# Kernel tuning notes

Measured on AMD Instinct MI355X. Metric: run time of the kernel, lower is better.

## Reference

```python
import jax, jax.numpy as jnp
import numpy as np

N, E = 50000, 800000
IN, HID, H, C = 128, 64, 4, 2
NEG_SLOPE = 0.2


def _gat_layer(h, src, dst, W, al, ar, b, out_dim, residual, resW=None, act='elu'):
    # h: [N, in]; W: [H*out, in]; al/ar: [H, out]; b: [H*out]
    n = h.shape[0]
    feat = (h @ W.T).reshape(n, H, out_dim)            # [N, H, out]
    el = jnp.einsum('nho,ho->nh', feat, al)            # [N, H]
    er = jnp.einsum('nho,ho->nh', feat, ar)            # [N, H]
    e = jax.nn.leaky_relu(el[src] + er[dst], NEG_SLOPE)  # [E, H]
    # segment softmax over incoming edges of each dst node
    emax = jax.ops.segment_max(e, dst, num_segments=n)
    ee = jnp.exp(e - emax[dst])
    denom = jax.ops.segment_sum(ee, dst, num_segments=n)
    alpha = ee / denom[dst]                             # [E, H]
    msg = feat[src] * alpha[:, :, None]                 # [E, H, out]
    rst = jax.ops.segment_sum(msg, dst, num_segments=n)  # [N, H, out]
    if residual == 'id':
        rst = rst + h.reshape(n, H, out_dim)
    elif residual == 'fc':
        rst = rst + (h @ resW.T).reshape(n, H, out_dim)
    rst = rst + b.reshape(1, H, out_dim)
    if act == 'elu':
        rst = jax.nn.elu(rst)
    else:  # softmax over last dim (F.softmax)
        rst = jax.nn.softmax(rst, axis=-1)
    return rst


def setup_inputs() -> dict:
    key = jax.random.key(0)
    ks = jax.random.split(key, 24)
    x = jax.random.normal(ks[0], (N, IN), dtype=jnp.float32)
    src = jax.random.randint(ks[1], (E,), 0, N)
    dst = jax.random.randint(ks[2], (E,), 0, N)
    s = 0.1
    d = {'x': x, 'src': src, 'dst': dst}
    # layer 1: IN -> (H, HID), no residual
    d['W1'] = jax.random.normal(ks[3], (H * HID, IN), dtype=jnp.float32) * s
    d['al1'] = jax.random.normal(ks[4], (H, HID), dtype=jnp.float32) * s
    d['ar1'] = jax.random.normal(ks[5], (H, HID), dtype=jnp.float32) * s
    d['b1'] = jnp.zeros((H * HID,), dtype=jnp.float32)
    # layers 2,3: H*HID -> (H, HID), identity residual
    d['W2'] = jax.random.normal(ks[6], (H * HID, H * HID), dtype=jnp.float32) * s
    d['al2'] = jax.random.normal(ks[7], (H, HID), dtype=jnp.float32) * s
    d['ar2'] = jax.random.normal(ks[8], (H, HID), dtype=jnp.float32) * s
    d['b2'] = jnp.zeros((H * HID,), dtype=jnp.float32)
    d['W3'] = jax.random.normal(ks[9], (H * HID, H * HID), dtype=jnp.float32) * s
    d['al3'] = jax.random.normal(ks[10], (H, HID), dtype=jnp.float32) * s
    d['ar3'] = jax.random.normal(ks[11], (H, HID), dtype=jnp.float32) * s
    d['b3'] = jnp.zeros((H * HID,), dtype=jnp.float32)
    # layer 4: H*HID -> (H, C), linear residual, softmax activation, mean over heads
    d['W4'] = jax.random.normal(ks[12], (H * C, H * HID), dtype=jnp.float32) * s
    d['al4'] = jax.random.normal(ks[13], (H, C), dtype=jnp.float32) * s
    d['ar4'] = jax.random.normal(ks[14], (H, C), dtype=jnp.float32) * s
    d['b4'] = jnp.zeros((H * C,), dtype=jnp.float32)
    d['resW4'] = jax.random.normal(ks[15], (H * C, H * HID), dtype=jnp.float32) * s
    return d


def reference(x, src, dst, W1, al1, ar1, b1, W2, al2, ar2, b2, W3, al3, ar3, b3, W4, al4, ar4, b4, resW4):
    h = _gat_layer(x, src, dst, W1, al1, ar1, b1, HID, 'none', act='elu').reshape(N, H * HID)
    h = _gat_layer(h, src, dst, W2, al2, ar2, b2, HID, 'id', act='elu').reshape(N, H * HID)
    h = _gat_layer(h, src, dst, W3, al3, ar3, b3, HID, 'id', act='elu').reshape(N, H * HID)
    h = _gat_layer(h, src, dst, W4, al4, ar4, b4, C, 'fc', resW=resW4, act='softmax')
    return h.mean(axis=1)  # [N, C]
```

## Files before the change

### kernel.cpp

```cpp
#include <hip/hip_runtime.h>
#include <hip/hip_bf16.h>
#include <math.h>


#define LEAKY_SLOPE 0.2f

typedef __bf16 bf16x8_t __attribute__((ext_vector_type(8)));
typedef float f32x4_t __attribute__((ext_vector_type(4)));
typedef float f32x2_t __attribute__((ext_vector_type(2)));

__device__ __forceinline__ float leaky(float x) { return x > 0.f ? x : LEAKY_SLOPE * x; }
__device__ __forceinline__ float eluf(float x)  { return x > 0.f ? x : expm1f(x); }
__device__ __forceinline__ float bflo(unsigned u) { return __uint_as_float(u << 16); }
__device__ __forceinline__ float bfhi(unsigned u) { return __uint_as_float(u & 0xffff0000u); }
__device__ __forceinline__ unsigned pk2(float a, float b) {
  __hip_bfloat162 t;
  t.x = __float2bfloat16(a);
  t.y = __float2bfloat16(b);
  return *(unsigned*)&t;
}

__device__ __forceinline__ float rlf(float v, int l) {
  return __uint_as_float((unsigned)__builtin_amdgcn_readlane((int)__float_as_uint(v), l));
}
template <int CTRL>
__device__ __forceinline__ float dpp_add(float x) {
  int t = __builtin_amdgcn_update_dpp(0, (int)__float_as_uint(x), CTRL, 0xf, 0xf, false);
  return x + __uint_as_float((unsigned)t);
}
__device__ __forceinline__ float wsum_dpp(float x) {
  x = dpp_add<0x111>(x);
  x = dpp_add<0x112>(x);
  x = dpp_add<0x114>(x);
  x = dpp_add<0x118>(x);
  x = dpp_add<0x142>(x);
  x = dpp_add<0x143>(x);
  return rlf(x, 63);
}
__device__ __forceinline__ float rowsum_dpp(float x) {
  x = dpp_add<0x111>(x);
  x = dpp_add<0x112>(x);
  x = dpp_add<0x114>(x);
  x = dpp_add<0x118>(x);
  return x;
}
__device__ __forceinline__ float wmax(float v) {
#pragma unroll
  for (int o = 32; o; o >>= 1) v = fmaxf(v, __shfl_xor(v, o));
  return v;
}
__device__ __forceinline__ float wsum_sh(float v) {
#pragma unroll
  for (int o = 32; o; o >>= 1) v += __shfl_xor(v, o);
  return v;
}

__device__ __forceinline__ void quad_fma(f32x2_t& a0, f32x2_t& a1, f32x2_t& a2, f32x2_t& a3,
                                         uint4 u, float w) {
  f32x2_t wv = {w, w};
  f32x2_t f;
  f[0] = bflo(u.x); f[1] = bfhi(u.x); a0 = __builtin_elementwise_fma(wv, f, a0);
  f[0] = bflo(u.y); f[1] = bfhi(u.y); a1 = __builtin_elementwise_fma(wv, f, a1);
  f[0] = bflo(u.z); f[1] = bfhi(u.z); a2 = __builtin_elementwise_fma(wv, f, a2);
  f[0] = bflo(u.w); f[1] = bfhi(u.w); a3 = __builtin_elementwise_fma(wv, f, a3);
}

__device__ __forceinline__ void gl_lds16(const __hip_bfloat16* g, __bf16* l) {
  __builtin_amdgcn_global_load_lds((const __attribute__((address_space(1))) void*)g,
                                   (__attribute__((address_space(3))) void*)l, 16, 0, 0);
}

__global__ __launch_bounds__(1024) void scan1_k(const int* __restrict__ deg,
                                                int* __restrict__ rowp,
                                                int* __restrict__ bsum, int n) {
  __shared__ int wtot[16];
  __shared__ int wpre[16];
  int tid = threadIdx.x, lane = tid & 63, wid = tid >> 6;
  int i = blockIdx.x * 1024 + tid;
  int v = (i < n) ? deg[i] : 0;
  int x = v;
#pragma unroll
  for (int off = 1; off < 64; off <<= 1) {
    int t = __shfl_up(x, off);
    if (lane >= off) x += t;
  }
  if (lane == 63) wtot[wid] = x;
  __syncthreads();
  if (wid == 0 && lane < 16) {
    int s = wtot[lane];
    int y = s;
#pragma unroll
    for (int off = 1; off < 16; off <<= 1) {
      int t = __shfl_up(y, off);
      if (lane >= off) y += t;
    }
    wpre[lane] = y - s;
    if (lane == 15) bsum[blockIdx.x] = y;
  }
  __syncthreads();
  if (i < n) rowp[i] = wpre[wid] + x - v;
}

__global__ void scan23_k(const int* __restrict__ bsum, int* __restrict__ rowp, int n, int nb) {
  __shared__ int pref[65];
  int tid = threadIdx.x;
  if (tid < 64) {
    int v = (tid < nb) ? bsum[tid] : 0;
    int x = v;
#pragma unroll
    for (int off = 1; off < 64; off <<= 1) {
      int t = __shfl_up(x, off);
      if (tid >= off) x += t;
    }
    pref[tid] = x - v;
    if (tid == 63) pref[64] = x;
  }
  __syncthreads();
  int i = blockIdx.x * 256 + tid;
  if (i < n) rowp[i] += pref[i >> 10];
  if (i == n) rowp[n] = pref[64];
}

__global__ void scatter_k(const int* __restrict__ src, const int* __restrict__ dst,
                          const int* __restrict__ rowp, int* __restrict__ cur,
                          int* __restrict__ csrc, int e) {
  int i = blockIdx.x * 256 + threadIdx.x;
  if (i < e) {
    int d = dst[i];
    int p = atomicAdd(&cur[d], 1);
    csrc[rowp[d] + p] = src[i];
  }
}

__global__ void cvthist_k(const float* __restrict__ x, const float* __restrict__ W1,
                          const float* __restrict__ W2, const float* __restrict__ W3,
                          const float* __restrict__ W4, const float* __restrict__ rW4,
                          __hip_bfloat16* __restrict__ xb, __hip_bfloat16* __restrict__ W1b,
                          __hip_bfloat16* __restrict__ W2b, __hip_bfloat16* __restrict__ W3b,
                          __hip_bfloat16* __restrict__ Wcatb, int nx4,
                          const int* __restrict__ dst, int* __restrict__ deg, int e) {
  int i = blockIdx.x * 256 + threadIdx.x;
  if (i < e) atomicAdd(&deg[dst[i]], 1);
  if (i < nx4) {
    float4 xv = ((const float4*)x)[i];
    uint2 o = {pk2(xv.x, xv.y), pk2(xv.z, xv.w)};
    ((uint2*)xb)[i] = o;
    return;
  }
  int j = i - nx4;
  const float* sp = nullptr;
  __hip_bfloat16* dp = nullptr;
  int idx = 0;
  if (j < 8192)       { sp = W1;  dp = W1b;          idx = j; }
  else if (j < 24576) { sp = W2;  dp = W2b;          idx = j - 8192; }
  else if (j < 40960) { sp = W3;  dp = W3b;          idx = j - 24576; }
  else if (j < 41472) { sp = W4;  dp = Wcatb;        idx = j - 40960; }
  else if (j < 41984) { sp = rW4; dp = Wcatb + 2048; idx = j - 41472; }
  else return;
  float4 wv = ((const float4*)sp)[idx];
  uint2 o = {pk2(wv.x, wv.y), pk2(wv.z, wv.w)};
  ((uint2*)dp)[idx] = o;
}

template <int K>
__global__ __launch_bounds__(256) void gemm_mfma(const __hip_bfloat16* __restrict__ A,
                                                 const __hip_bfloat16* __restrict__ B,
                                                 __hip_bfloat16* __restrict__ featb,
                                                 const float* __restrict__ al,
                                                 const float* __restrict__ ar,
                                                 float* __restrict__ el,
                                                 float* __restrict__ er, int n, int nbx) {
  __shared__ __bf16 As[2][128 * 32];
  __shared__ __bf16 Bs[2][128 * 32];
  const int wg = blockIdx.x;
  const int b = ((wg >> 4) << 3) + (wg & 7);
  if (b >= nbx) return;
  const int cb = (wg >> 3) & 1;
  const int r0 = b * 128, c0 = cb * 128;

  const int tid = threadIdx.x;
  const int lane = tid & 63, w = tid >> 6;
  const int tm = lane & 15, tq = lane >> 4;
  const int wm = (w & 1) * 64, wn = (w >> 1) * 64;

  f32x4_t acc[4][4];
#pragma unroll
  for (int i = 0; i < 4; ++i)
#pragma unroll
    for (int j = 0; j < 4; ++j) acc[i][j] = 0.f;

  const bool interior = (r0 + 128 <= n);
  if (interior) {
    const int srow = w * 32 + (lane >> 2);
    const int scol = (lane & 3) * 8;
    const __hip_bfloat16* ga0 = A + (size_t)(r0 + srow) * K + scol;
    const __hip_bfloat16* gb0 = B + (size_t)(c0 + srow) * K + scol;
    for (int kk = 0; kk < K; kk += 64) {
      const __hip_bfloat16* ga = ga0 + kk;
      const __hip_bfloat16* gb = gb0 + kk;
      __syncthreads();
      gl_lds16(ga, &As[0][w * 1024]);
      gl_lds16(ga + (size_t)16 * K, &As[0][w * 1024 + 512]);
      gl_lds16(ga + 32, &As[1][w * 1024]);
      gl_lds16(ga + (size_t)16 * K + 32, &As[1][w * 1024 + 512]);
      gl_lds16(gb, &Bs[0][w * 1024]);
      gl_lds16(gb + (size_t)16 * K, &Bs[0][w * 1024 + 512]);
      gl_lds16(gb + 32, &Bs[1][w * 1024]);
      gl_lds16(gb + (size_t)16 * K + 32, &Bs[1][w * 1024 + 512]);
      __syncthreads();
#pragma unroll
      for (int ks = 0; ks < 2; ++ks) {
        bf16x8_t af[4], bfr[4];
#pragma unroll
        for (int i = 0; i < 4; ++i)
          af[i] = *(const bf16x8_t*)&As[ks][(wm + i * 16 + tm) * 32 + tq * 8];
#pragma unroll
        for (int j = 0; j < 4; ++j)
          bfr[j] = *(const bf16x8_t*)&Bs[ks][(wn + j * 16 + tm) * 32 + tq * 8];
#pragma unroll
        for (int i = 0; i < 4; ++i)
#pragma unroll
          for (int j = 0; j < 4; ++j)
            acc[i][j] = __builtin_amdgcn_mfma_f32_16x16x32_bf16(af[i], bfr[j], acc[i][j], 0, 0, 0);
      }
    }
  } else {
    const int srow = tid >> 1, sko = (tid & 1) * 16;
    for (int kk = 0; kk < K; kk += 32) {
      uint4 av0 = {0, 0, 0, 0}, av1 = {0, 0, 0, 0};
      int arw = r0 + srow;
      if (arw < n) {
        const uint4* p = (const uint4*)(A + (size_t)arw * K + kk + sko);
        av0 = p[0];
        av1 = p[1];
      }
      const uint4* q = (const uint4*)(B + (size_t)(c0 + srow) * K + kk + sko);
      uint4 bv0 = q[0], bv1 = q[1];
      __syncthreads();
      *(uint4*)&As[0][srow * 32 + sko] = av0;
      *(uint4*)&As[0][srow * 32 + sko + 8] = av1;
      *(uint4*)&Bs[0][srow * 32 + sko] = bv0;
      *(uint4*)&Bs[0][srow * 32 + sko + 8] = bv1;
      __syncthreads();
      bf16x8_t af[4], bfr[4];
#pragma unroll
      for (int i = 0; i < 4; ++i)
        af[i] = *(const bf16x8_t*)&As[0][(wm + i * 16 + tm) * 32 + tq * 8];
#pragma unroll
      for (int j = 0; j < 4; ++j)
        bfr[j] = *(const bf16x8_t*)&Bs[0][(wn + j * 16 + tm) * 32 + tq * 8];
#pragma unroll
      for (int i = 0; i < 4; ++i)
#pragma unroll
        for (int j = 0; j < 4; ++j)
          acc[i][j] = __builtin_amdgcn_mfma_f32_16x16x32_bf16(af[i], bfr[j], acc[i][j], 0, 0, 0);
    }
  }

#pragma unroll
  for (int i = 0; i < 4; ++i) {
#pragma unroll
    for (int j = 0; j < 4; ++j) {
      int col = c0 + wn + j * 16 + tm;
#pragma unroll
      for (int rr = 0; rr < 4; ++rr) {
        int row = r0 + wm + i * 16 + tq * 4 + rr;
        if (row < n) featb[(size_t)row * 256 + col] = __float2bfloat16(acc[i][j][rr]);
      }
    }
  }

  {
    const int hd = (c0 + wn) >> 6;
    float alv[4], arv[4];
#pragma unroll
    for (int j = 0; j < 4; ++j) {
      alv[j] = al[hd * 64 + j * 16 + tm];
      arv[j] = ar[hd * 64 + j * 16 + tm];
    }
#pragma unroll
    for (int i = 0; i < 4; ++i) {
#pragma unroll
      for (int rr = 0; rr < 4; ++rr) {
        float se = acc[i][0][rr] * alv[0] + acc[i][1][rr] * alv[1] +
                   acc[i][2][rr] * alv[2] + acc[i][3][rr] * alv[3];
        float sr2 = acc[i][0][rr] * arv[0] + acc[i][1][rr] * arv[1] +
                    acc[i][2][rr] * arv[2] + acc[i][3][rr] * arv[3];
        se = rowsum_dpp(se);
        sr2 = rowsum_dpp(sr2);
        if (tm == 15) {
          int row = r0 + wm + i * 16 + tq * 4 + rr;
          if (row < n) {
            el[(size_t)row * 4 + hd] = se;
            er[(size_t)row * 4 + hd] = sr2;
          }
        }
      }
    }
  }
}

template <int RES>
__global__ __launch_bounds__(256) void agg64_k(const __hip_bfloat16* __restrict__ featb,
                                               const float* __restrict__ el,
                                               const float* __restrict__ er,
                                               const int* __restrict__ rowp,
                                               const int* __restrict__ csrc,
                                               const __hip_bfloat16* __restrict__ hinb,
                                               const float* __restrict__ bias,
                                               __hip_bfloat16* __restrict__ houtb, int n) {
  __shared__ float wsh[4][256];
  __shared__ int ssh[4][64];
  int wv = threadIdx.x >> 6;
  int node = blockIdx.x * 4 + wv;
  int lane = threadIdx.x & 63;
  if (node >= n) return;
  int s0 = rowp[node], s1 = rowp[node + 1];
  int deg = s1 - s0;
  float4 erv = *(const float4*)(er + (size_t)node * 4);

  if (deg <= 64) {
    int sown = 0;
    float x0 = 0.f, x1 = 0.f, x2 = 0.f, x3 = 0.f;
    if (lane < deg) {
      sown = csrc[s0 + lane];
      float4 e = *(const float4*)(el + (size_t)sown * 4);
      x0 = __expf(leaky(e.x + erv.x));
      x1 = __expf(leaky(e.y + erv.y));
      x2 = __expf(leaky(e.z + erv.z));
      x3 = __expf(leaky(e.w + erv.w));
    }
    float d0 = wsum_dpp(x0), d1 = wsum_dpp(x1), d2 = wsum_dpp(x2), d3 = wsum_dpp(x3);
    float i0 = d0 > 0.f ? 1.f / d0 : 0.f;
    float i1 = d1 > 0.f ? 1.f / d1 : 0.f;
    float i2 = d2 > 0.f ? 1.f / d2 : 0.f;
    float i3 = d3 > 0.f ? 1.f / d3 : 0.f;
    float4 wq = {x0 * i0, x1 * i1, x2 * i2, x3 * i3};
    *(float4*)&wsh[wv][lane * 4] = wq;
    ssh[wv][lane] = sown;

    const int half = lane >> 5, sub = lane & 31;
    const int hh = sub >> 3;
    f32x2_t a0 = {0.f, 0.f}, a1 = {0.f, 0.f}, a2 = {0.f, 0.f}, a3 = {0.f, 0.f};
    const int G = deg >> 3;
    int k = 0;
    if (G) {
      int ke = half;
      int sk0 = ssh[wv][ke], sk1 = ssh[wv][ke + 2];
      int sk2 = ssh[wv][ke + 4], sk3 = ssh[wv][ke + 6];
      uint4 u0 = ((const uint4*)(featb + ((size_t)sk0 << 8)))[sub];
      uint4 u1 = ((const uint4*)(featb + ((size_t)sk1 << 8)))[sub];
      uint4 u2 = ((const uint4*)(featb + ((size_t)sk2 << 8)))[sub];
      uint4 u3 = ((const uint4*)(featb + ((size_t)sk3 << 8)))[sub];
      float w0 = wsh[wv][ke * 4 + hh];
      float w1 = wsh[wv][(ke + 2) * 4 + hh];
      float w2 = wsh[wv][(ke + 4) * 4 + hh];
      float w3 = wsh[wv][(ke + 6) * 4 + hh];
      for (int g = 1; g < G; ++g) {
        int kb = g * 8 + half;
        int t0 = ssh[wv][kb], t1 = ssh[wv][kb + 2];
        int t2 = ssh[wv][kb + 4], t3 = ssh[wv][kb + 6];
        uint4 v0 = ((const uint4*)(featb + ((size_t)t0 << 8)))[sub];
        uint4 v1 = ((const uint4*)(featb + ((size_t)t1 << 8)))[sub];
        uint4 v2 = ((const uint4*)(featb + ((size_t)t2 << 8)))[sub];
        uint4 v3 = ((const uint4*)(featb + ((size_t)t3 << 8)))[sub];
        float y0 = wsh[wv][kb * 4 + hh];
        float y1 = wsh[wv][(kb + 2) * 4 + hh];
        float y2 = wsh[wv][(kb + 4) * 4 + hh];
        float y3 = wsh[wv][(kb + 6) * 4 + hh];
        quad_fma(a0, a1, a2, a3, u0, w0);
        quad_fma(a0, a1, a2, a3, u1, w1);
        quad_fma(a0, a1, a2, a3, u2, w2);
        quad_fma(a0, a1, a2, a3, u3, w3);
        u0 = v0; u1 = v1; u2 = v2; u3 = v3;
        w0 = y0; w1 = y1; w2 = y2; w3 = y3;
      }
      quad_fma(a0, a1, a2, a3, u0, w0);
      quad_fma(a0, a1, a2, a3, u1, w1);
      quad_fma(a0, a1, a2, a3, u2, w2);
      quad_fma(a0, a1, a2, a3, u3, w3);
      k = G * 8;
    }
    for (; k < deg; k += 2) {
      int ke = k + half;
      int sk = ssh[wv][ke];
      uint4 u = ((const uint4*)(featb + ((size_t)sk << 8)))[sub];
      float wk = wsh[wv][ke * 4 + hh];
      quad_fma(a0, a1, a2, a3, u, wk);
    }
    a0[0] += __shfl_xor(a0[0], 32); a0[1] += __shfl_xor(a0[1], 32);
    a1[0] += __shfl_xor(a1[0], 32); a1[1] += __shfl_xor(a1[1], 32);
    a2[0] += __shfl_xor(a2[0], 32); a2[1] += __shfl_xor(a2[1], 32);
    a3[0] += __shfl_xor(a3[0], 32); a3[1] += __shfl_xor(a3[1], 32);

    if (half == 0) {
      size_t base = (size_t)node * 256 + sub * 8;
      float v0 = a0[0], v1 = a0[1], v2 = a1[0], v3 = a1[1];
      float v4 = a2[0], v5 = a2[1], v6 = a3[0], v7 = a3[1];
      float4 b0 = *(const float4*)(bias + sub * 8);
      float4 b1 = *(const float4*)(bias + sub * 8 + 4);
      v0 += b0.x; v1 += b0.y; v2 += b0.z; v3 += b0.w;
      v4 += b1.x; v5 += b1.y; v6 += b1.z; v7 += b1.w;
      if (RES) {
        uint4 r = *(const uint4*)(hinb + base);
        v0 += bflo(r.x); v1 += bfhi(r.x);
        v2 += bflo(r.y); v3 += bfhi(r.y);
        v4 += bflo(r.z); v5 += bfhi(r.z);
        v6 += bflo(r.w); v7 += bfhi(r.w);
      }
      uint4 o;
      o.x = pk2(eluf(v0), eluf(v1));
      o.y = pk2(eluf(v2), eluf(v3));
      o.z = pk2(eluf(v4), eluf(v5));
      o.w = pk2(eluf(v6), eluf(v7));
      *(uint4*)(houtb + base) = o;
    }
  } else {
    int hsel = lane >> 4;
    f32x2_t a01 = {0.f, 0.f}, a23 = {0.f, 0.f};
    float m0 = -INFINITY, m1 = -INFINITY, m2 = -INFINITY, m3 = -INFINITY;
    for (int k = s0 + lane; k < s1; k += 64) {
      int s = csrc[k];
      float4 e = *(const float4*)(el + (size_t)s * 4);
      m0 = fmaxf(m0, leaky(e.x + erv.x));
      m1 = fmaxf(m1, leaky(e.y + erv.y));
      m2 = fmaxf(m2, leaky(e.z + erv.z));
      m3 = fmaxf(m3, leaky(e.w + erv.w));
    }
    m0 = wmax(m0); m1 = wmax(m1); m2 = wmax(m2); m3 = wmax(m3);
    float d0 = 0, d1 = 0, d2 = 0, d3 = 0;
    for (int k = s0 + lane; k < s1; k += 64) {
      int s = csrc[k];
      float4 e = *(const float4*)(el + (size_t)s * 4);
      d0 += __expf(leaky(e.x + erv.x) - m0);
      d1 += __expf(leaky(e.y + erv.y) - m1);
      d2 += __expf(leaky(e.z + erv.z) - m2);
      d3 += __expf(leaky(e.w + erv.w) - m3);
    }
    d0 = wsum_sh(d0); d1 = wsum_sh(d1); d2 = wsum_sh(d2); d3 = wsum_sh(d3);
    float j0 = d0 > 0.f ? 1.f / d0 : 0.f;
    float j1 = d1 > 0.f ? 1.f / d1 : 0.f;
    float j2 = d2 > 0.f ? 1.f / d2 : 0.f;
    float j3 = d3 > 0.f ? 1.f / d3 : 0.f;
    for (int k = s0; k < s1; ++k) {
      int s = csrc[k];
      float4 e = *(const float4*)(el + (size_t)s * 4);
      float w0 = __expf(leaky(e.x + erv.x) - m0) * j0;
      float w1 = __expf(leaky(e.y + erv.y) - m1) * j1;
      float w2 = __expf(leaky(e.z + erv.z) - m2) * j2;
      float w3 = __expf(leaky(e.w + erv.w) - m3) * j3;
      float wk = (hsel == 0) ? w0 : (hsel == 1) ? w1 : (hsel == 2) ? w2 : w3;
      uint2 u = ((const uint2*)(featb + ((size_t)s << 8)))[lane];
      f32x2_t wv2 = {wk, wk};
      f32x2_t f;
      f[0] = bflo(u.x); f[1] = bfhi(u.x); a01 = __builtin_elementwise_fma(wv2, f, a01);
      f[0] = bflo(u.y); f[1] = bfhi(u.y); a23 = __builtin_elementwise_fma(wv2, f, a23);
    }
    size_t base = (size_t)node * 256 + lane * 4;
    float4 bv = *(const float4*)(bias + lane * 4);
    float v0 = a01[0] + bv.x, v1 = a01[1] + bv.y;
    float v2 = a23[0] + bv.z, v3 = a23[1] + bv.w;
    if (RES) {
      uint2 r = *(const uint2*)(hinb + base);
      v0 += bflo(r.x); v1 += bfhi(r.x);
      v2 += bflo(r.y); v3 += bfhi(r.y);
    }
    uint2 o;
    o.x = pk2(eluf(v0), eluf(v1));
    o.y = pk2(eluf(v2), eluf(v3));
    *(uint2*)(houtb + base) = o;
  }
}

__global__ __launch_bounds__(256) void l4mfma_k(const __hip_bfloat16* __restrict__ hb,
                                                const __hip_bfloat16* __restrict__ Wcat,
                                                const float* __restrict__ al4,
                                                const float* __restrict__ ar4,
                                                float* __restrict__ feat4,
                                                float* __restrict__ res4,
                                                float* __restrict__ el4,
                                                float* __restrict__ er4, int n) {
  int wid = blockIdx.x * 4 + (threadIdx.x >> 6);
  int n16 = (n + 15) >> 4;
  if (wid >= n16) return;
  int lane = threadIdx.x & 63;
  int tm = lane & 15, tq = lane >> 4;
  int row = wid * 16 + tm;
  int rowc = row < n ? row : n - 1;
  const __hip_bfloat16* ap = hb + (size_t)rowc * 256 + tq * 8;
  const __hip_bfloat16* bp = Wcat + (size_t)tm * 256 + tq * 8;
  f32x4_t acc = {0.f, 0.f, 0.f, 0.f};
#pragma unroll
  for (int k = 0; k < 8; ++k) {
    bf16x8_t af = *(const bf16x8_t*)(ap + k * 32);
    bf16x8_t bf = *(const bf16x8_t*)(bp + k * 32);
    acc = __builtin_amdgcn_mfma_f32_16x16x32_bf16(af, bf, acc, 0, 0, 0);
  }
  float* dstp = (tm < 8) ? feat4 : res4;
  int cc = tm & 7;
  float a4 = (tm < 8) ? al4[tm] : 0.f;
  float r4 = (tm < 8) ? ar4[tm] : 0.f;
#pragma unroll
  for (int r = 0; r < 4; ++r) {
    int node = wid * 16 + tq * 4 + r;
    float te = acc[r] * a4;
    float tr = acc[r] * r4;
    te += __shfl_xor(te, 1);
    tr += __shfl_xor(tr, 1);
    if (node < n) {
      dstp[(size_t)node * 8 + cc] = acc[r];
      if (tm < 8 && (tm & 1) == 0) {
        el4[(size_t)node * 4 + (tm >> 1)] = te;
        er4[(size_t)node * 4 + (tm >> 1)] = tr;
      }
    }
  }
}

__global__ __launch_bounds__(256) void agg4_k(const float* __restrict__ feat4,
                                              const float* __restrict__ el4,
                                              const float* __restrict__ er4,
                                              const int* __restrict__ rowp,
                                              const int* __restrict__ csrc,
                                              const float* __restrict__ res4,
                                              const float* __restrict__ b4,
                                              float* __restrict__ out, int n) {
  int wv = threadIdx.x >> 6;
  int node = blockIdx.x * 4 + wv;
  int lane = threadIdx.x & 63;
  if (node >= n) return;
  int s0 = rowp[node], s1 = rowp[node + 1];
  int deg = s1 - s0;
  float4 erv = *(const float4*)(er4 + (size_t)node * 4);
  float v = 0.f;

  if (deg <= 64) {
    int sown = 0;
    float x0 = 0.f, x1 = 0.f, x2 = 0.f, x3 = 0.f;
    if (lane < deg) {
      sown = csrc[s0 + lane];
      float4 e = *(const float4*)(el4 + (size_t)sown * 4);
      x0 = __expf(leaky(e.x + erv.x));
      x1 = __expf(leaky(e.y + erv.y));
      x2 = __expf(leaky(e.z + erv.z));
      x3 = __expf(leaky(e.w + erv.w));
    }
    float d0 = wsum_dpp(x0), d1 = wsum_dpp(x1), d2 = wsum_dpp(x2), d3 = wsum_dpp(x3);
    float w0 = x0 * (d0 > 0.f ? 1.f / d0 : 0.f);
    float w1 = x1 * (d1 > 0.f ? 1.f / d1 : 0.f);
    float w2 = x2 * (d2 > 0.f ? 1.f / d2 : 0.f);
    float w3 = x3 * (d3 > 0.f ? 1.f / d3 : 0.f);
    float4 f0 = {0, 0, 0, 0}, f1 = {0, 0, 0, 0};
    if (lane < deg) {
      const float4* fp = (const float4*)(feat4 + (size_t)sown * 8);
      f0 = fp[0];
      f1 = fp[1];
    }
    float t0 = w0 * f0.x, t1 = w0 * f0.y;
    float t2 = w1 * f0.z, t3 = w1 * f0.w;
    float t4 = w2 * f1.x, t5 = w2 * f1.y;
    float t6 = w3 * f1.z, t7 = w3 * f1.w;
    t0 = wsum_dpp(t0); t1 = wsum_dpp(t1); t2 = wsum_dpp(t2); t3 = wsum_dpp(t3);
    t4 = wsum_dpp(t4); t5 = wsum_dpp(t5); t6 = wsum_dpp(t6); t7 = wsum_dpp(t7);
    int p = lane & 7;
    float s = t0;
    s = (p == 1) ? t1 : s; s = (p == 2) ? t2 : s; s = (p == 3) ? t3 : s;
    s = (p == 4) ? t4 : s; s = (p == 5) ? t5 : s; s = (p == 6) ? t6 : s;
    s = (p == 7) ? t7 : s;
    if (lane < 8) v = s + res4[(size_t)node * 8 + lane] + b4[lane];
  } else {
    int p = lane & 7, hh = p >> 1;
    float acc = 0.f;
    float m0 = -INFINITY, m1 = -INFINITY, m2 = -INFINITY, m3 = -INFINITY;
    for (int k = s0 + lane; k < s1; k += 64) {
      int s = csrc[k];
      float4 e = *(const float4*)(el4 + (size_t)s * 4);
      m0 = fmaxf(m0, leaky(e.x + erv.x));
      m1 = fmaxf(m1, leaky(e.y + erv.y));
      m2 = fmaxf(m2, leaky(e.z + erv.z));
      m3 = fmaxf(m3, leaky(e.w + erv.w));
    }
    m0 = wmax(m0); m1 = wmax(m1); m2 = wmax(m2); m3 = wmax(m3);
    float d0 = 0, d1 = 0, d2 = 0, d3 = 0;
    for (int k = s0 + lane; k < s1; k += 64) {
      int s = csrc[k];
      float4 e = *(const float4*)(el4 + (size_t)s * 4);
      d0 += __expf(leaky(e.x + erv.x) - m0);
      d1 += __expf(leaky(e.y + erv.y) - m1);
      d2 += __expf(leaky(e.z + erv.z) - m2);
      d3 += __expf(leaky(e.w + erv.w) - m3);
    }
    d0 = wsum_sh(d0); d1 = wsum_sh(d1); d2 = wsum_sh(d2); d3 = wsum_sh(d3);
    float i0 = d0 > 0.f ? 1.f / d0 : 0.f;
    float i1 = d1 > 0.f ? 1.f / d1 : 0.f;
    float i2 = d2 > 0.f ? 1.f / d2 : 0.f;
    float i3 = d3 > 0.f ? 1.f / d3 : 0.f;
    for (int k = s0; k < s1; ++k) {
      int s = csrc[k];
      float4 e = *(const float4*)(el4 + (size_t)s * 4);
      float w0 = __expf(leaky(e.x + erv.x) - m0) * i0;
      float w1 = __expf(leaky(e.y + erv.y) - m1) * i1;
      float w2 = __expf(leaky(e.z + erv.z) - m2) * i2;
      float w3 = __expf(leaky(e.w + erv.w) - m3) * i3;
      float wk = (hh == 0) ? w0 : (hh == 1) ? w1 : (hh == 2) ? w2 : w3;
      if (lane < 8) acc = fmaf(wk, feat4[(size_t)s * 8 + p], acc);
    }
    if (lane < 8) v = acc + res4[(size_t)node * 8 + lane] + b4[lane];
  }

  float pv = __shfl_xor(v, 1);
  float mx = fmaxf(v, pv);
  float ex = __expf(v - mx);
  float sm = ex + __shfl_xor(ex, 1);
  float pr = ex / sm;
  float t = pr + __shfl_xor(pr, 2);
  t += __shfl_xor(t, 4);
  if (lane < 2) out[(size_t)node * 2 + lane] = t * 0.25f;
}

extern "C" void kernel_launch(void* const* d_in, const int* in_sizes, int n_in,
                              void* d_out, int out_size, void* d_ws, size_t ws_size,
                              hipStream_t stream) {
  const float* x   = (const float*)d_in[0];
  const int* src   = (const int*)d_in[1];
  const int* dst   = (const int*)d_in[2];
  const float* W1  = (const float*)d_in[3];
  const float* al1 = (const float*)d_in[4];
  const float* ar1 = (const float*)d_in[5];
  const float* b1  = (const float*)d_in[6];
  const float* W2  = (const float*)d_in[7];
  const float* al2 = (const float*)d_in[8];
  const float* ar2 = (const float*)d_in[9];
  const float* b2  = (const float*)d_in[10];
  const float* W3  = (const float*)d_in[11];
  const float* al3 = (const float*)d_in[12];
  const float* ar3 = (const float*)d_in[13];
  const float* b3  = (const float*)d_in[14];
  const float* W4  = (const float*)d_in[15];
  const float* al4 = (const float*)d_in[16];
  const float* ar4 = (const float*)d_in[17];
  const float* b4  = (const float*)d_in[18];
  const float* rW4 = (const float*)d_in[19];
  float* out = (float*)d_out;

  const int n = in_sizes[0] / 128;
  const int e = in_sizes[1];

  char* ws = (char*)d_ws;
  auto alloc = [&](size_t bytes) -> char* {
    char* p = ws;
    ws += (bytes + 255) & ~(size_t)255;
    return p;
  };
  __hip_bfloat16* featb = (__hip_bfloat16*)alloc((size_t)n * 256 * 2);
  __hip_bfloat16* h1b   = (__hip_bfloat16*)alloc((size_t)n * 256 * 2);
  __hip_bfloat16* h2b   = (__hip_bfloat16*)alloc((size_t)n * 256 * 2);
  __hip_bfloat16* h3b   = (__hip_bfloat16*)alloc((size_t)n * 256 * 2);
  __hip_bfloat16* xb    = (__hip_bfloat16*)alloc((size_t)n * 128 * 2);
  __hip_bfloat16* W1b   = (__hip_bfloat16*)alloc((size_t)256 * 128 * 2);
  __hip_bfloat16* W2b   = (__hip_bfloat16*)alloc((size_t)256 * 256 * 2);
  __hip_bfloat16* W3b   = (__hip_bfloat16*)alloc((size_t)256 * 256 * 2);
  __hip_bfloat16* Wcatb = (__hip_bfloat16*)alloc((size_t)16 * 256 * 2);
  float* el    = (float*)alloc((size_t)n * 4 * 4);
  float* er    = (float*)alloc((size_t)n * 4 * 4);
  float* feat4 = (float*)alloc((size_t)n * 8 * 4);
  float* res4  = (float*)alloc((size_t)n * 8 * 4);
  float* el4   = (float*)alloc((size_t)n * 4 * 4);
  float* er4   = (float*)alloc((size_t)n * 4 * 4);
  int* deg     = (int*)alloc((size_t)2 * n * 4);
  int* cur     = deg + n;
  int* rowp    = (int*)alloc((size_t)(n + 1) * 4);
  int* csrc    = (int*)alloc((size_t)e * 4);
  int nb_scan  = (n + 1023) / 1024;
  int* bsum    = (int*)alloc((size_t)(nb_scan + 1) * 4);

  (void)hipMemsetAsync(deg, 0, (size_t)2 * n * 4, stream);

  int nx4 = n * 128 / 4;
  int nwork = nx4 + 41984;
  if (nwork < e) nwork = e;
  cvthist_k<<<(nwork + 255) / 256, 256, 0, stream>>>(x, W1, W2, W3, W4, rW4, xb, W1b,
                                                     W2b, W3b, Wcatb, nx4, dst, deg, e);
  scan1_k<<<nb_scan, 1024, 0, stream>>>(deg, rowp, bsum, n);
  scan23_k<<<(n + 256) / 256, 256, 0, stream>>>(bsum, rowp, n, nb_scan);
  scatter_k<<<(e + 255) / 256, 256, 0, stream>>>(src, dst, rowp, cur, csrc, e);

  int nbx = (n + 127) / 128;
  int ggx = ((2 * nbx + 15) / 16) * 16;
  int nb4 = (n + 3) / 4;

  gemm_mfma<128><<<ggx, 256, 0, stream>>>(xb, W1b, featb, al1, ar1, el, er, n, nbx);
  agg64_k<0><<<nb4, 256, 0, stream>>>(featb, el, er, rowp, csrc, nullptr, b1, h1b, n);
  gemm_mfma<256><<<ggx, 256, 0, stream>>>(h1b, W2b, featb, al2, ar2, el, er, n, nbx);
  agg64_k<1><<<nb4, 256, 0, stream>>>(featb, el, er, rowp, csrc, h1b, b2, h2b, n);
  gemm_mfma<256><<<ggx, 256, 0, stream>>>(h2b, W3b, featb, al3, ar3, el, er, n, nbx);
  agg64_k<1><<<nb4, 256, 0, stream>>>(featb, el, er, rowp, csrc, h2b, b3, h3b, n);
  int n16 = (n + 15) / 16;
  l4mfma_k<<<(n16 + 3) / 4, 256, 0, stream>>>(h3b, Wcatb, al4, ar4, feat4, res4, el4, er4, n);
  agg4_k<<<nb4, 256, 0, stream>>>(feat4, el4, er4, rowp, csrc, res4, b4, out, n);
}
```

Measured before the change: 474.6 us.

## Fuse x fp32-to-bf16 conversion into layer-1 GEMM and record CSR slots in histogram

Layer 1's GEMM now reads x in fp32 directly, converting it to bf16 while staging into shared memory. This removes the separate pass that wrote a bf16 copy of x and the extra read of that copy. The histogram kernel also saves each edge's atomic return value as a slot index, so the scatter kernel needs no second atomic pass and only half as much counter memory is zeroed. The cost is a new per-edge slot array, plus A-tile loads in the new GEMM that are synchronous and single-buffered instead of async.

```diff
diff --git a/kernel.cpp b/kernel.cpp
--- a/kernel.cpp
+++ b/kernel.cpp
@@ -122,44 +122,164 @@
 }
 
 __global__ void scatter_k(const int* __restrict__ src, const int* __restrict__ dst,
-                          const int* __restrict__ rowp, int* __restrict__ cur,
+                          const int* __restrict__ rowp, const int* __restrict__ slot,
                           int* __restrict__ csrc, int e) {
   int i = blockIdx.x * 256 + threadIdx.x;
+  if (i < e) csrc[rowp[dst[i]] + slot[i]] = src[i];
+}
+
+__global__ void cvthist_k(const float* __restrict__ W1, const float* __restrict__ W2,
+                          const float* __restrict__ W3, const float* __restrict__ W4,
+                          const float* __restrict__ rW4,
+                          __hip_bfloat16* __restrict__ W1b, __hip_bfloat16* __restrict__ W2b,
+                          __hip_bfloat16* __restrict__ W3b, __hip_bfloat16* __restrict__ Wcatb,
+                          const int* __restrict__ dst, int* __restrict__ deg,
+                          int* __restrict__ slot, int e) {
+  int i = blockIdx.x * 256 + threadIdx.x;
   if (i < e) {
-    int d = dst[i];
-    int p = atomicAdd(&cur[d], 1);
-    csrc[rowp[d] + p] = src[i];
-  }
-}
-
-__global__ void cvthist_k(const float* __restrict__ x, const float* __restrict__ W1,
-                          const float* __restrict__ W2, const float* __restrict__ W3,
-                          const float* __restrict__ W4, const float* __restrict__ rW4,
-                          __hip_bfloat16* __restrict__ xb, __hip_bfloat16* __restrict__ W1b,
-                          __hip_bfloat16* __restrict__ W2b, __hip_bfloat16* __restrict__ W3b,
-                          __hip_bfloat16* __restrict__ Wcatb, int nx4,
-                          const int* __restrict__ dst, int* __restrict__ deg, int e) {
-  int i = blockIdx.x * 256 + threadIdx.x;
-  if (i < e) atomicAdd(&deg[dst[i]], 1);
-  if (i < nx4) {
-    float4 xv = ((const float4*)x)[i];
-    uint2 o = {pk2(xv.x, xv.y), pk2(xv.z, xv.w)};
-    ((uint2*)xb)[i] = o;
-    return;
-  }
-  int j = i - nx4;
-  const float* sp = nullptr;
-  __hip_bfloat16* dp = nullptr;
-  int idx = 0;
-  if (j < 8192)       { sp = W1;  dp = W1b;          idx = j; }
-  else if (j < 24576) { sp = W2;  dp = W2b;          idx = j - 8192; }
-  else if (j < 40960) { sp = W3;  dp = W3b;          idx = j - 24576; }
-  else if (j < 41472) { sp = W4;  dp = Wcatb;        idx = j - 40960; }
-  else if (j < 41984) { sp = rW4; dp = Wcatb + 2048; idx = j - 41472; }
-  else return;
-  float4 wv = ((const float4*)sp)[idx];
-  uint2 o = {pk2(wv.x, wv.y), pk2(wv.z, wv.w)};
-  ((uint2*)dp)[idx] = o;
+    int p = atomicAdd(&deg[dst[i]], 1);
+    slot[i] = p;
+  }
+  if (i < 41984) {
+    const float* sp;
+    __hip_bfloat16* dp;
+    int idx;
+    if (i < 8192)       { sp = W1;  dp = W1b;          idx = i; }
+    else if (i < 24576) { sp = W2;  dp = W2b;          idx = i - 8192; }
+    else if (i < 40960) { sp = W3;  dp = W3b;          idx = i - 24576; }
+    else if (i < 41472) { sp = W4;  dp = Wcatb;        idx = i - 40960; }
+    else                { sp = rW4; dp = Wcatb + 2048; idx = i - 41472; }
+    float4 wv = ((const float4*)sp)[idx];
+    uint2 o = {pk2(wv.x, wv.y), pk2(wv.z, wv.w)};
+    ((uint2*)dp)[idx] = o;
+  }
+}
+
+__global__ __launch_bounds__(256) void gemm1f_mfma(const float* __restrict__ A,
+                                                   const __hip_bfloat16* __restrict__ B,
+                                                   __hip_bfloat16* __restrict__ featb,
+                                                   const float* __restrict__ al,
+                                                   const float* __restrict__ ar,
+                                                   float* __restrict__ el,
+                                                   float* __restrict__ er, int n, int nbx) {
+  __shared__ __bf16 As[2][128 * 32];
+  __shared__ __bf16 Bs[2][128 * 32];
+  const int wg = blockIdx.x;
+  const int b = ((wg >> 4) << 3) + (wg & 7);
+  if (b >= nbx) return;
+  const int cb = (wg >> 3) & 1;
+  const int r0 = b * 128, c0 = cb * 128;
+
+  const int tid = threadIdx.x;
+  const int lane = tid & 63, w = tid >> 6;
+  const int tm = lane & 15, tq = lane >> 4;
+  const int wm = (w & 1) * 64, wn = (w >> 1) * 64;
+
+  f32x4_t acc[4][4];
+#pragma unroll
+  for (int i = 0; i < 4; ++i)
+#pragma unroll
+    for (int j = 0; j < 4; ++j) acc[i][j] = 0.f;
+
+  const int srow = tid >> 1;
+  const int sh = tid & 1;
+  const int arw = r0 + srow;
+  const bool aok = arw < n;
+  const float* ap = A + (size_t)arw * 128 + sh * 32;
+
+  const int srB = w * 32 + (lane >> 2);
+  const int scB = (lane & 3) * 8;
+  const __hip_bfloat16* gb0 = B + (size_t)(c0 + srB) * 128 + scB;
+
+#pragma unroll
+  for (int kk = 0; kk < 128; kk += 64) {
+    float4 av0 = {0, 0, 0, 0}, av1 = {0, 0, 0, 0}, av2 = {0, 0, 0, 0}, av3 = {0, 0, 0, 0};
+    float4 av4 = {0, 0, 0, 0}, av5 = {0, 0, 0, 0}, av6 = {0, 0, 0, 0}, av7 = {0, 0, 0, 0};
+    if (aok) {
+      const float4* p = (const float4*)(ap + kk);
+      av0 = p[0]; av1 = p[1]; av2 = p[2]; av3 = p[3];
+      av4 = p[4]; av5 = p[5]; av6 = p[6]; av7 = p[7];
+    }
+    __syncthreads();
+    const __hip_bfloat16* gbk = gb0 + kk;
+    gl_lds16(gbk, &Bs[0][w * 1024]);
+    gl_lds16(gbk + (size_t)16 * 128, &Bs[0][w * 1024 + 512]);
+    gl_lds16(gbk + 32, &Bs[1][w * 1024]);
+    gl_lds16(gbk + (size_t)16 * 128 + 32, &Bs[1][w * 1024 + 512]);
+    {
+      uint4 o;
+      o.x = pk2(av0.x, av0.y); o.y = pk2(av0.z, av0.w);
+      o.z = pk2(av1.x, av1.y); o.w = pk2(av1.z, av1.w);
+      *(uint4*)&As[sh][srow * 32 + 0] = o;
+      o.x = pk2(av2.x, av2.y); o.y = pk2(av2.z, av2.w);
+      o.z = pk2(av3.x, av3.y); o.w = pk2(av3.z, av3.w);
+      *(uint4*)&As[sh][srow * 32 + 8] = o;
+      o.x = pk2(av4.x, av4.y); o.y = pk2(av4.z, av4.w);
+      o.z = pk2(av5.x, av5.y); o.w = pk2(av5.z, av5.w);
+      *(uint4*)&As[sh][srow * 32 + 16] = o;
+      o.x = pk2(av6.x, av6.y); o.y = pk2(av6.z, av6.w);
+      o.z = pk2(av7.x, av7.y); o.w = pk2(av7.z, av7.w);
+      *(uint4*)&As[sh][srow * 32 + 24] = o;
+    }
+    __syncthreads();
+#pragma unroll
+    for (int ks = 0; ks < 2; ++ks) {
+      bf16x8_t af[4], bfr[4];
+#pragma unroll
+      for (int i = 0; i < 4; ++i)
+        af[i] = *(const bf16x8_t*)&As[ks][(wm + i * 16 + tm) * 32 + tq * 8];
+#pragma unroll
+      for (int j = 0; j < 4; ++j)
+        bfr[j] = *(const bf16x8_t*)&Bs[ks][(wn + j * 16 + tm) * 32 + tq * 8];
+#pragma unroll
+      for (int i = 0; i < 4; ++i)
+#pragma unroll
+        for (int j = 0; j < 4; ++j)
+          acc[i][j] = __builtin_amdgcn_mfma_f32_16x16x32_bf16(af[i], bfr[j], acc[i][j], 0, 0, 0);
+    }
+  }
+
+#pragma unroll
+  for (int i = 0; i < 4; ++i) {
+#pragma unroll
+    for (int j = 0; j < 4; ++j) {
+      int col = c0 + wn + j * 16 + tm;
+#pragma unroll
+      for (int rr = 0; rr < 4; ++rr) {
+        int row = r0 + wm + i * 16 + tq * 4 + rr;
+        if (row < n) featb[(size_t)row * 256 + col] = __float2bfloat16(acc[i][j][rr]);
+      }
+    }
+  }
+
+  {
+    const int hd = (c0 + wn) >> 6;
+    float alv[4], arv[4];
+#pragma unroll
+    for (int j = 0; j < 4; ++j) {
+      alv[j] = al[hd * 64 + j * 16 + tm];
+      arv[j] = ar[hd * 64 + j * 16 + tm];
+    }
+#pragma unroll
+    for (int i = 0; i < 4; ++i) {
+#pragma unroll
+      for (int rr = 0; rr < 4; ++rr) {
+        float se = acc[i][0][rr] * alv[0] + acc[i][1][rr] * alv[1] +
+                   acc[i][2][rr] * alv[2] + acc[i][3][rr] * alv[3];
+        float sr2 = acc[i][0][rr] * arv[0] + acc[i][1][rr] * arv[1] +
+                    acc[i][2][rr] * arv[2] + acc[i][3][rr] * arv[3];
+        se = rowsum_dpp(se);
+        sr2 = rowsum_dpp(sr2);
+        if (tm == 15) {
+          int row = r0 + wm + i * 16 + tq * 4 + rr;
+          if (row < n) {
+            el[(size_t)row * 4 + hd] = se;
+            er[(size_t)row * 4 + hd] = sr2;
+          }
+        }
+      }
+    }
+  }
 }
 
 template <int K>
@@ -656,7 +776,6 @@
   __hip_bfloat16* h1b   = (__hip_bfloat16*)alloc((size_t)n * 256 * 2);
   __hip_bfloat16* h2b   = (__hip_bfloat16*)alloc((size_t)n * 256 * 2);
   __hip_bfloat16* h3b   = (__hip_bfloat16*)alloc((size_t)n * 256 * 2);
-  __hip_bfloat16* xb    = (__hip_bfloat16*)alloc((size_t)n * 128 * 2);
   __hip_bfloat16* W1b   = (__hip_bfloat16*)alloc((size_t)256 * 128 * 2);
   __hip_bfloat16* W2b   = (__hip_bfloat16*)alloc((size_t)256 * 256 * 2);
   __hip_bfloat16* W3b   = (__hip_bfloat16*)alloc((size_t)256 * 256 * 2);
@@ -667,29 +786,26 @@
   float* res4  = (float*)alloc((size_t)n * 8 * 4);
   float* el4   = (float*)alloc((size_t)n * 4 * 4);
   float* er4   = (float*)alloc((size_t)n * 4 * 4);
-  int* deg     = (int*)alloc((size_t)2 * n * 4);
-  int* cur     = deg + n;
+  int* deg     = (int*)alloc((size_t)n * 4);
   int* rowp    = (int*)alloc((size_t)(n + 1) * 4);
   int* csrc    = (int*)alloc((size_t)e * 4);
+  int* slot    = (int*)alloc((size_t)e * 4);
   int nb_scan  = (n + 1023) / 1024;
   int* bsum    = (int*)alloc((size_t)(nb_scan + 1) * 4);
 
-  (void)hipMemsetAsync(deg, 0, (size_t)2 * n * 4, stream);
-
-  int nx4 = n * 128 / 4;
-  int nwork = nx4 + 41984;
-  if (nwork < e) nwork = e;
-  cvthist_k<<<(nwork + 255) / 256, 256, 0, stream>>>(x, W1, W2, W3, W4, rW4, xb, W1b,
-                                                     W2b, W3b, Wcatb, nx4, dst, deg, e);
+  (void)hipMemsetAsync(deg, 0, (size_t)n * 4, stream);
+
+  cvthist_k<<<(e + 255) / 256, 256, 0, stream>>>(W1, W2, W3, W4, rW4, W1b, W2b, W3b,
+                                                 Wcatb, dst, deg, slot, e);
   scan1_k<<<nb_scan, 1024, 0, stream>>>(deg, rowp, bsum, n);
   scan23_k<<<(n + 256) / 256, 256, 0, stream>>>(bsum, rowp, n, nb_scan);
-  scatter_k<<<(e + 255) / 256, 256, 0, stream>>>(src, dst, rowp, cur, csrc, e);
+  scatter_k<<<(e + 255) / 256, 256, 0, stream>>>(src, dst, rowp, slot, csrc, e);
 
   int nbx = (n + 127) / 128;
   int ggx = ((2 * nbx + 15) / 16) * 16;
   int nb4 = (n + 3) / 4;
 
-  gemm_mfma<128><<<ggx, 256, 0, stream>>>(xb, W1b, featb, al1, ar1, el, er, n, nbx);
+  gemm1f_mfma<<<ggx, 256, 0, stream>>>(x, W1b, featb, al1, ar1, el, er, n, nbx);
   agg64_k<0><<<nb4, 256, 0, stream>>>(featb, el, er, rowp, csrc, nullptr, b1, h1b, n);
   gemm_mfma<256><<<ggx, 256, 0, stream>>>(h1b, W2b, featb, al2, ar2, el, er, n, nbx);
   agg64_k<1><<<nb4, 256, 0, stream>>>(featb, el, er, rowp, csrc, h1b, b2, h2b, n);
```

Result: faster. 449.6 us (-5.3%).
